# Optimization experiments

Hardware: AMD Instinct MI355X
Metric: run time of the kernel (lower is better)

Reference implementation:

```python
import math
import jax, jax.numpy as jnp
import numpy as np

B, NQ, NKV, D, H = 32, 512, 512, 1024, 8
DH = D // H              # 128
N_COLS = 512             # n + 1
D_COL = math.ceil(2 * math.log2(N_COLS))  # 18


def setup_inputs() -> dict:
    key = jax.random.key(0)
    ks = jax.random.split(key, 8)
    s = 0.02
    return {
        "x_q": jax.random.normal(ks[0], (B, NQ, D), jnp.float32),
        "x_kv": jax.random.normal(ks[1], (B, NKV, D), jnp.float32),
        # sym_weight=True => W_tail is W_head (shared)
        "W_head_w": jax.random.normal(ks[2], (D, D), jnp.float32) * s,
        "W_head_b": jnp.zeros((D,), jnp.float32),
        "W_v_w": jax.random.normal(ks[3], (D, D), jnp.float32) * s,
        "W_v_b": jnp.zeros((D,), jnp.float32),
        "W_out_w": jax.random.normal(ks[4], (D, D), jnp.float32) * s,
        "W_out_b": jnp.zeros((D,), jnp.float32),
        "rel_emb": jnp.ones((H, DH), jnp.float32),
        "col_head": jax.random.normal(ks[5], (H, N_COLS, D_COL), jnp.float32) * 0.2,
        "col_tail": jax.random.normal(ks[6], (H, N_COLS, D_COL), jnp.float32) * 0.2,
    }


def _heads(x, W, b, h, dh):
    # Linear then split heads: [B, n, d] -> [B, H, n, dh]
    B_, n, _ = x.shape
    y = x @ W.T + b
    return y.reshape(B_, n, h, dh).transpose(0, 2, 1, 3)


def reference(x_q, x_kv, W_head_w, W_head_b, W_v_w, W_v_b,
              W_out_w, W_out_b, rel_emb, col_head, col_tail):
    Bb, nq, d = x_q.shape
    nkv = x_kv.shape[1]
    h, dh = rel_emb.shape

    f_head = _heads(x_q, W_head_w, W_head_b, h, dh) * rel_emb[None, :, None, :]
    f_tail = _heads(x_kv, W_head_w, W_head_b, h, dh) * rel_emb[None, :, None, :]  # W_tail = W_head (sym_weight)
    f_v = _heads(x_kv, W_v_w, W_v_b, h, dh)

    # content score: [B, H, nq, nkv]
    weight_score = jnp.einsum('bhqd,bhkd->bhqk', f_head, f_tail) / math.sqrt(dh)

    # learned column topology: [H, n_cols, n_cols]
    adj_logits = jnp.einsum('hqc,hkc->hqk', col_head, col_tail)
    eye = jnp.eye(adj_logits.shape[-1], dtype=bool)  # nsi: zero diagonal before softmax
    adj_logits = jnp.where(eye[None], 0.0, adj_logits)
    adj = jax.nn.softmax(adj_logits, axis=-1)[:, :nq, :nkv]

    adj_mask = (1.0 - adj) * -10000.0
    fr_graph = jax.nn.softmax(weight_score + adj_mask[None], axis=-1)

    x = jnp.einsum('bhqk,bhkd->bhqd', fr_graph, f_v)
    x = x.transpose(0, 2, 1, 3).reshape(Bb, nq, h * dh)
    x = x @ W_out_w.T + W_out_b
    return (x, fr_graph.reshape(Bb * h, nq, nkv))
```

## Files before the change

kernel.cpp:

```cpp
#include <hip/hip_runtime.h>

typedef __attribute__((ext_vector_type(8))) __bf16 bf8;
typedef __attribute__((ext_vector_type(4))) __bf16 bf4;
typedef __attribute__((ext_vector_type(4))) float f32x4;

#define DEVI static __device__ __forceinline__

DEVI void gload_lds16(const void* g, void* l) {
  __builtin_amdgcn_global_load_lds(
      (const __attribute__((address_space(1))) unsigned int*)g,
      (__attribute__((address_space(3))) unsigned int*)l, 16, 0, 0);
}

#define WAITV(N)                                             \
  asm volatile("s_waitcnt vmcnt(" #N ")" ::: "memory");      \
  __builtin_amdgcn_sched_barrier(0)
#define BARRIER()                      \
  __builtin_amdgcn_sched_barrier(0);   \
  __builtin_amdgcn_s_barrier();        \
  __builtin_amdgcn_sched_barrier(0)

__global__ __launch_bounds__(256) void cvt_kernel(const float* __restrict__ in,
                                                  __bf16* __restrict__ out, int n4) {
  int stride = gridDim.x * blockDim.x;
  for (int i = blockIdx.x * blockDim.x + threadIdx.x; i < n4; i += stride) {
    f32x4 v = reinterpret_cast<const f32x4*>(in)[i];
    bf4 o;
    o[0] = (__bf16)v[0]; o[1] = (__bf16)v[1]; o[2] = (__bf16)v[2]; o[3] = (__bf16)v[3];
    reinterpret_cast<bf4*>(out)[i] = o;
  }
}

template <int MODE>
__global__ __launch_bounds__(512, 2) void gemm_proj(
    const __bf16* __restrict__ A, const __bf16* __restrict__ Bw,
    const float* __restrict__ bias, const float* __restrict__ rel,
    __bf16* __restrict__ obf, float* __restrict__ of32) {
  __shared__ alignas(16) __bf16 As0[256 * 64];
  __shared__ alignas(16) __bf16 Bs0[256 * 64];
  __shared__ alignas(16) __bf16 As1[256 * 64];
  __shared__ alignas(16) __bf16 Bs1[256 * 64];
  const int tid = threadIdx.x;
  const int lane = tid & 63;
  const int wave = tid >> 6;
  const int wr = wave >> 2;
  const int wc = wave & 3;
  const int lr = lane & 15;
  const int khi = lane >> 4;
  const int bm = blockIdx.x, bn = blockIdx.y;

  const __bf16* Ab = A + (size_t)bm * 256 * 1024;
  const __bf16* Bb = Bw + (size_t)bn * 256 * 1024;

  const int srow = tid >> 3;
  const int scc = (tid & 7) ^ (srow & 7);

  f32x4 acc[8][4];
#pragma unroll
  for (int mi = 0; mi < 8; ++mi)
#pragma unroll
    for (int ni = 0; ni < 4; ++ni)
#pragma unroll
      for (int e = 0; e < 4; ++e) acc[mi][ni][e] = 0.f;

  auto STAGE = [&](const __bf16* gb, __bf16* lds, int kt) {
#pragma unroll
    for (int i = 0; i < 4; ++i)
      gload_lds16(gb + (size_t)(i * 64 + srow) * 1024 + kt * 64 + scc * 8,
                  lds + i * 4096 + tid * 8);
  };

  auto COMPUTE = [&](const __bf16* As, const __bf16* Bs) {
    __builtin_amdgcn_s_setprio(1);
#pragma unroll
    for (int kk = 0; kk < 2; ++kk) {
      const int ck = ((kk * 4 + khi) ^ (lr & 7)) * 8;
      bf8 a[8], b[4];
#pragma unroll
      for (int mi = 0; mi < 8; ++mi)
        a[mi] = *reinterpret_cast<const bf8*>(&As[(wr * 128 + mi * 16 + lr) * 64 + ck]);
#pragma unroll
      for (int ni = 0; ni < 4; ++ni)
        b[ni] = *reinterpret_cast<const bf8*>(&Bs[(wc * 64 + ni * 16 + lr) * 64 + ck]);
#pragma unroll
      for (int mi = 0; mi < 8; ++mi)
#pragma unroll
        for (int ni = 0; ni < 4; ++ni)
          acc[mi][ni] = __builtin_amdgcn_mfma_f32_16x16x32_bf16(a[mi], b[ni], acc[mi][ni], 0, 0, 0);
    }
    __builtin_amdgcn_s_setprio(0);
  };

  STAGE(Ab, As0, 0); STAGE(Bb, Bs0, 0);
  STAGE(Ab, As1, 1); STAGE(Bb, Bs1, 1);

  for (int it = 0; it < 7; ++it) {
    WAITV(8);
    BARRIER();
    COMPUTE(As0, Bs0);
    BARRIER();
    STAGE(Ab, As0, 2 * it + 2); STAGE(Bb, Bs0, 2 * it + 2);
    WAITV(8);
    BARRIER();
    COMPUTE(As1, Bs1);
    BARRIER();
    STAGE(Ab, As1, 2 * it + 3); STAGE(Bb, Bs1, 2 * it + 3);
  }
  WAITV(8);
  BARRIER();
  COMPUTE(As0, Bs0);
  WAITV(0);
  BARRIER();
  COMPUTE(As1, Bs1);

#pragma unroll
  for (int mi = 0; mi < 8; ++mi) {
#pragma unroll
    for (int ni = 0; ni < 4; ++ni) {
      const int n = bn * 256 + wc * 64 + ni * 16 + lr;
#pragma unroll
      for (int r = 0; r < 4; ++r) {
        const int m = bm * 256 + wr * 128 + mi * 16 + khi * 4 + r;
        float v = acc[mi][ni][r] + bias[n];
        if (MODE == 0) v *= rel[n];
        if (MODE == 2) {
          of32[(size_t)m * 1024 + n] = v;
        } else if (MODE == 0) {
          size_t idx = ((size_t)((m >> 9) * 8 + (n >> 7))) * 65536 +
                       (size_t)(m & 511) * 128 + (n & 127);
          obf[idx] = (__bf16)v;
        } else {
          size_t idx = ((size_t)((m >> 9) * 8 + (n >> 7))) * 65536 +
                       (size_t)(n & 127) * 512 + (m & 511);
          obf[idx] = (__bf16)v;
        }
      }
    }
  }
}

__global__ __launch_bounds__(256) void adj_kernel(const float* __restrict__ ch_all,
                                                  const float* __restrict__ ct_all,
                                                  __bf16* __restrict__ adjT) {
  const int wave = threadIdx.x >> 6, lane = threadIdx.x & 63;
  const int row = blockIdx.x * 4 + wave;
  const int h = row >> 9, i = row & 511;
  float ch[18];
  const float* chp = ch_all + ((size_t)h * 512 + i) * 18;
#pragma unroll
  for (int t = 0; t < 18; ++t) ch[t] = chp[t];
  float e[8];
  float m = -1e30f;
#pragma unroll
  for (int jj = 0; jj < 8; ++jj) {
    const int j = jj * 64 + lane;
    const float* ctp = ct_all + ((size_t)h * 512 + j) * 18;
    float d = 0.f;
#pragma unroll
    for (int t = 0; t < 18; ++t) d += ch[t] * ctp[t];
    if (j == i) d = 0.f;
    e[jj] = d;
    m = fmaxf(m, d);
  }
#pragma unroll
  for (int off = 32; off >= 1; off >>= 1) m = fmaxf(m, __shfl_xor(m, off));
  float s = 0.f;
#pragma unroll
  for (int jj = 0; jj < 8; ++jj) { e[jj] = __expf(e[jj] - m); s += e[jj]; }
#pragma unroll
  for (int off = 32; off >= 1; off >>= 1) s += __shfl_xor(s, off);
  const float inv = 10000.f / s;
  __bf16* op = adjT + (size_t)h * 262144 + i;
#pragma unroll
  for (int jj = 0; jj < 8; ++jj)
    op[(size_t)(jj * 64 + lane) * 512] = (__bf16)(e[jj] * inv - 19.53125f);
}

__global__ __launch_bounds__(256, 3) void fused_attn_kernel(
    const __bf16* __restrict__ fh, const __bf16* __restrict__ ft,
    const __bf16* __restrict__ fvT, const __bf16* __restrict__ adjT,
    float* __restrict__ fr, __bf16* __restrict__ ctx) {
  __shared__ alignas(16) __bf16 Bt[128 * 128];
  __shared__ alignas(16) __bf16 Pl[4][16 * 128];
  const int tid = threadIdx.x;
  const int l = tid & 63, w = tid >> 6;
  const int b = blockIdx.x;
  const int h = blockIdx.y >> 3;
  const int qt = blockIdx.y & 7;
  const int bh = b * 8 + h;
  const int wrow = qt * 64 + w * 16;
  const int lr = l & 15;
  const int khi = l >> 4;

  const int srow = tid >> 4;
  const int scc = (tid & 15) ^ (srow & 7);

  bf8 afr[4];
  {
    const __bf16* ap = fh + (size_t)bh * 65536 + (size_t)(wrow + lr) * 128 + khi * 8;
#pragma unroll
    for (int kk4 = 0; kk4 < 4; ++kk4)
      afr[kk4] = *reinterpret_cast<const bf8*>(ap + kk4 * 32);
  }

  f32x4 acc[32];
#pragma unroll
  for (int n = 0; n < 32; ++n)
#pragma unroll
    for (int e = 0; e < 4; ++e) acc[n][e] = 0.f;

  const __bf16* ftb = ft + (size_t)bh * 65536;
#pragma unroll
  for (int kt = 0; kt < 4; ++kt) {
#pragma unroll
    for (int i = 0; i < 8; ++i)
      gload_lds16(ftb + (size_t)(kt * 128 + i * 16 + srow) * 128 + scc * 8,
                  Bt + i * 2048 + tid * 8);
    __syncthreads();
    __builtin_amdgcn_s_setprio(1);
#pragma unroll
    for (int kk4 = 0; kk4 < 4; ++kk4) {
      bf8 bfr[8];
#pragma unroll
      for (int n2 = 0; n2 < 8; ++n2)
        bfr[n2] = *reinterpret_cast<const bf8*>(
            &Bt[(n2 * 16 + lr) * 128 + ((kk4 * 4 + khi) ^ (lr & 7)) * 8]);
#pragma unroll
      for (int n2 = 0; n2 < 8; ++n2)
        acc[kt * 8 + n2] =
            __builtin_amdgcn_mfma_f32_16x16x32_bf16(afr[kk4], bfr[n2], acc[kt * 8 + n2], 0, 0, 0);
    }
    __builtin_amdgcn_s_setprio(0);
    __syncthreads();
  }

  const float scale = 0.08838834764831845f;
  const __bf16* adjTp = adjT + (size_t)h * 262144;
  float mrow[4] = {-1e30f, -1e30f, -1e30f, -1e30f};
#pragma unroll
  for (int n = 0; n < 32; ++n) {
    const int col = n * 16 + lr;
    bf4 av4 = *reinterpret_cast<const bf4*>(adjTp + (size_t)col * 512 + wrow + khi * 4);
#pragma unroll
    for (int r = 0; r < 4; ++r) {
      float v = acc[n][r] * scale + (float)av4[r];
      acc[n][r] = v;
      mrow[r] = fmaxf(mrow[r], v);
    }
  }
#pragma unroll
  for (int r = 0; r < 4; ++r)
#pragma unroll
    for (int off = 1; off <= 8; off <<= 1) mrow[r] = fmaxf(mrow[r], __shfl_xor(mrow[r], off));
  float srw[4] = {0.f, 0.f, 0.f, 0.f};
#pragma unroll
  for (int n = 0; n < 32; ++n)
#pragma unroll
    for (int r = 0; r < 4; ++r) {
      float e = __expf(acc[n][r] - mrow[r]);
      acc[n][r] = e;
      srw[r] += e;
    }
#pragma unroll
  for (int r = 0; r < 4; ++r)
#pragma unroll
    for (int off = 1; off <= 8; off <<= 1) srw[r] += __shfl_xor(srw[r], off);
  float inv[4];
#pragma unroll
  for (int r = 0; r < 4; ++r) inv[r] = 1.f / srw[r];
#pragma unroll
  for (int n = 0; n < 32; ++n)
#pragma unroll
    for (int r = 0; r < 4; ++r) acc[n][r] *= inv[r];

  const __bf16* fvb = fvT + (size_t)bh * 65536;
#pragma unroll
  for (int i = 0; i < 8; ++i)
    gload_lds16(fvb + (size_t)(i * 16 + srow) * 512 + scc * 8, Bt + i * 2048 + tid * 8);

  {
    float* frb = fr + (size_t)bh * 262144;
#pragma unroll
    for (int n = 0; n < 32; ++n) {
      const int col = n * 16 + lr;
#pragma unroll
      for (int r = 0; r < 4; ++r)
        frb[(size_t)(wrow + khi * 4 + r) * 512 + col] = acc[n][r];
    }
  }

  f32x4 acc2[8];
#pragma unroll
  for (int n2 = 0; n2 < 8; ++n2)
#pragma unroll
    for (int e = 0; e < 4; ++e) acc2[n2][e] = 0.f;

  __bf16* Pw = &Pl[w][0];
#pragma unroll
  for (int kt = 0; kt < 4; ++kt) {
#pragma unroll
    for (int n2 = 0; n2 < 8; ++n2) {
      const int colc = n2 * 2 + (lr >> 3);
      const int cl = lr & 7;
#pragma unroll
      for (int r = 0; r < 4; ++r) {
        const int q = khi * 4 + r;
        Pw[q * 128 + ((colc ^ (q & 7)) * 8) + cl] = (__bf16)acc[kt * 8 + n2][r];
      }
    }
    __syncthreads();
    __builtin_amdgcn_s_setprio(1);
#pragma unroll
    for (int kk4 = 0; kk4 < 4; ++kk4) {
      bf8 pa = *reinterpret_cast<const bf8*>(
          &Pw[lr * 128 + ((kk4 * 4 + khi) ^ (lr & 7)) * 8]);
      bf8 bfr[8];
#pragma unroll
      for (int n2 = 0; n2 < 8; ++n2)
        bfr[n2] = *reinterpret_cast<const bf8*>(
            &Bt[(n2 * 16 + lr) * 128 + ((kk4 * 4 + khi) ^ (lr & 7)) * 8]);
#pragma unroll
      for (int n2 = 0; n2 < 8; ++n2)
        acc2[n2] = __builtin_amdgcn_mfma_f32_16x16x32_bf16(pa, bfr[n2], acc2[n2], 0, 0, 0);
    }
    __builtin_amdgcn_s_setprio(0);
    __syncthreads();
    if (kt < 3) {
      const int ktn = kt + 1;
#pragma unroll
      for (int i = 0; i < 8; ++i)
        gload_lds16(fvb + (size_t)(i * 16 + srow) * 512 + ktn * 128 + scc * 8,
                    Bt + i * 2048 + tid * 8);
    }
  }

#pragma unroll
  for (int n2 = 0; n2 < 8; ++n2) {
    const int c = n2 * 16 + lr;
#pragma unroll
    for (int r = 0; r < 4; ++r) {
      const int q = wrow + khi * 4 + r;
      ctx[(size_t)(b * 512 + q) * 1024 + h * 128 + c] = (__bf16)acc2[n2][r];
    }
  }
}

extern "C" void kernel_launch(void* const* d_in, const int* in_sizes, int n_in,
                              void* d_out, int out_size, void* d_ws, size_t ws_size,
                              hipStream_t stream) {
  const float* x_q  = (const float*)d_in[0];
  const float* x_kv = (const float*)d_in[1];
  const float* Wh   = (const float*)d_in[2];
  const float* bh   = (const float*)d_in[3];
  const float* Wv   = (const float*)d_in[4];
  const float* bv   = (const float*)d_in[5];
  const float* Wo   = (const float*)d_in[6];
  const float* bo   = (const float*)d_in[7];
  const float* rel  = (const float*)d_in[8];
  const float* colh = (const float*)d_in[9];
  const float* colt = (const float*)d_in[10];

  float* out = (float*)d_out;
  float* fr  = out + 16777216;

  __bf16* xq_bf  = (__bf16*)d_ws;
  __bf16* xkv_bf = xq_bf + 16777216;
  __bf16* Wh_bf  = xkv_bf + 16777216;
  __bf16* Wv_bf  = Wh_bf + 1048576;
  __bf16* Wo_bf  = Wv_bf + 1048576;
  __bf16* fhead  = Wo_bf + 1048576;
  __bf16* ftail  = fhead + 16777216;
  __bf16* fvT    = ftail + 16777216;
  __bf16* adjT   = fvT + 16777216;
  __bf16* ctx    = adjT + 2097152;

  cvt_kernel<<<4096, 256, 0, stream>>>(x_q, xq_bf, 4194304);
  cvt_kernel<<<4096, 256, 0, stream>>>(x_kv, xkv_bf, 4194304);
  cvt_kernel<<<1024, 256, 0, stream>>>(Wh, Wh_bf, 262144);
  cvt_kernel<<<1024, 256, 0, stream>>>(Wv, Wv_bf, 262144);
  cvt_kernel<<<1024, 256, 0, stream>>>(Wo, Wo_bf, 262144);

  dim3 gp(64, 4);
  gemm_proj<0><<<gp, 512, 0, stream>>>(xq_bf, Wh_bf, bh, rel, fhead, nullptr);
  gemm_proj<0><<<gp, 512, 0, stream>>>(xkv_bf, Wh_bf, bh, rel, ftail, nullptr);
  gemm_proj<1><<<gp, 512, 0, stream>>>(xkv_bf, Wv_bf, bv, nullptr, fvT, nullptr);

  adj_kernel<<<1024, 256, 0, stream>>>(colh, colt, adjT);

  fused_attn_kernel<<<dim3(32, 64), 256, 0, stream>>>(fhead, ftail, fvT, adjT, fr, ctx);

  gemm_proj<2><<<gp, 512, 0, stream>>>(ctx, Wo_bf, bo, nullptr, nullptr, out);
}
```

Measured before the change: 817.1 us.

## Double-buffer LDS staging of K and V tiles in fused attention kernel

Splits the single shared-memory tile into two buffers. Each K/V tile load is issued one stage ahead, and the first V tiles are prefetched during the QK^T loop. Full `__syncthreads` calls are replaced with explicit vmcnt/lgkmcnt waits and barriers, so global-to-LDS copies overlap MFMA work. This costs extra LDS, which cuts the launch-bounds occupancy target from 3 to 2 blocks per CU. The vmcnt waits also now cover the fr output stores issued before the PV loop.

```diff
diff --git a/kernel.cpp b/kernel.cpp
--- a/kernel.cpp
+++ b/kernel.cpp
@@ -14,6 +14,9 @@
 
 #define WAITV(N)                                             \
   asm volatile("s_waitcnt vmcnt(" #N ")" ::: "memory");      \
+  __builtin_amdgcn_sched_barrier(0)
+#define LGKM0()                                              \
+  asm volatile("s_waitcnt lgkmcnt(0)" ::: "memory");         \
   __builtin_amdgcn_sched_barrier(0)
 #define BARRIER()                      \
   __builtin_amdgcn_sched_barrier(0);   \
@@ -176,11 +179,12 @@
     op[(size_t)(jj * 64 + lane) * 512] = (__bf16)(e[jj] * inv - 19.53125f);
 }
 
-__global__ __launch_bounds__(256, 3) void fused_attn_kernel(
+__global__ __launch_bounds__(256, 2) void fused_attn_kernel(
     const __bf16* __restrict__ fh, const __bf16* __restrict__ ft,
     const __bf16* __restrict__ fvT, const __bf16* __restrict__ adjT,
     float* __restrict__ fr, __bf16* __restrict__ ctx) {
-  __shared__ alignas(16) __bf16 Bt[128 * 128];
+  __shared__ alignas(16) __bf16 Bt0[128 * 128];
+  __shared__ alignas(16) __bf16 Bt1[128 * 128];
   __shared__ alignas(16) __bf16 Pl[4][16 * 128];
   const int tid = threadIdx.x;
   const int l = tid & 63, w = tid >> 6;
@@ -203,20 +207,35 @@
       afr[kk4] = *reinterpret_cast<const bf8*>(ap + kk4 * 32);
   }
 
-  f32x4 acc[32];
-#pragma unroll
-  for (int n = 0; n < 32; ++n)
-#pragma unroll
-    for (int e = 0; e < 4; ++e) acc[n][e] = 0.f;
-
   const __bf16* ftb = ft + (size_t)bh * 65536;
-#pragma unroll
-  for (int kt = 0; kt < 4; ++kt) {
+  const __bf16* fvb = fvT + (size_t)bh * 65536;
+
+  auto stage_ft = [&](__bf16* dst, int kt) {
 #pragma unroll
     for (int i = 0; i < 8; ++i)
       gload_lds16(ftb + (size_t)(kt * 128 + i * 16 + srow) * 128 + scc * 8,
-                  Bt + i * 2048 + tid * 8);
-    __syncthreads();
+                  dst + i * 2048 + tid * 8);
+  };
+  auto stage_fv = [&](__bf16* dst, int kt) {
+#pragma unroll
+    for (int i = 0; i < 8; ++i)
+      gload_lds16(fvb + (size_t)(i * 16 + srow) * 512 + kt * 128 + scc * 8,
+                  dst + i * 2048 + tid * 8);
+  };
+
+  f32x4 acc[32];
+#pragma unroll
+  for (int n = 0; n < 32; ++n)
+#pragma unroll
+    for (int e = 0; e < 4; ++e) acc[n][e] = 0.f;
+
+  stage_ft(Bt0, 0);
+  stage_ft(Bt1, 1);
+#pragma unroll
+  for (int kt = 0; kt < 4; ++kt) {
+    __bf16* B = (kt & 1) ? Bt1 : Bt0;
+    WAITV(8);
+    BARRIER();
     __builtin_amdgcn_s_setprio(1);
 #pragma unroll
     for (int kk4 = 0; kk4 < 4; ++kk4) {
@@ -224,14 +243,18 @@
 #pragma unroll
       for (int n2 = 0; n2 < 8; ++n2)
         bfr[n2] = *reinterpret_cast<const bf8*>(
-            &Bt[(n2 * 16 + lr) * 128 + ((kk4 * 4 + khi) ^ (lr & 7)) * 8]);
+            &B[(n2 * 16 + lr) * 128 + ((kk4 * 4 + khi) ^ (lr & 7)) * 8]);
 #pragma unroll
       for (int n2 = 0; n2 < 8; ++n2)
         acc[kt * 8 + n2] =
             __builtin_amdgcn_mfma_f32_16x16x32_bf16(afr[kk4], bfr[n2], acc[kt * 8 + n2], 0, 0, 0);
     }
     __builtin_amdgcn_s_setprio(0);
-    __syncthreads();
+    BARRIER();
+    if (kt == 0) stage_ft(Bt0, 2);
+    else if (kt == 1) stage_ft(Bt1, 3);
+    else if (kt == 2) stage_fv(Bt0, 0);
+    else stage_fv(Bt1, 1);
   }
 
   const float scale = 0.08838834764831845f;
@@ -273,11 +296,6 @@
 #pragma unroll
     for (int r = 0; r < 4; ++r) acc[n][r] *= inv[r];
 
-  const __bf16* fvb = fvT + (size_t)bh * 65536;
-#pragma unroll
-  for (int i = 0; i < 8; ++i)
-    gload_lds16(fvb + (size_t)(i * 16 + srow) * 512 + scc * 8, Bt + i * 2048 + tid * 8);
-
   {
     float* frb = fr + (size_t)bh * 262144;
 #pragma unroll
@@ -298,6 +316,7 @@
   __bf16* Pw = &Pl[w][0];
 #pragma unroll
   for (int kt = 0; kt < 4; ++kt) {
+    __bf16* B = (kt & 1) ? Bt1 : Bt0;
 #pragma unroll
     for (int n2 = 0; n2 < 8; ++n2) {
       const int colc = n2 * 2 + (lr >> 3);
@@ -308,7 +327,9 @@
         Pw[q * 128 + ((colc ^ (q & 7)) * 8) + cl] = (__bf16)acc[kt * 8 + n2][r];
       }
     }
-    __syncthreads();
+    LGKM0();
+    if (kt < 3) { WAITV(8); } else { WAITV(0); }
+    BARRIER();
     __builtin_amdgcn_s_setprio(1);
 #pragma unroll
     for (int kk4 = 0; kk4 < 4; ++kk4) {
@@ -318,19 +339,16 @@
 #pragma unroll
       for (int n2 = 0; n2 < 8; ++n2)
         bfr[n2] = *reinterpret_cast<const bf8*>(
-            &Bt[(n2 * 16 + lr) * 128 + ((kk4 * 4 + khi) ^ (lr & 7)) * 8]);
+            &B[(n2 * 16 + lr) * 128 + ((kk4 * 4 + khi) ^ (lr & 7)) * 8]);
 #pragma unroll
       for (int n2 = 0; n2 < 8; ++n2)
         acc2[n2] = __builtin_amdgcn_mfma_f32_16x16x32_bf16(pa, bfr[n2], acc2[n2], 0, 0, 0);
     }
     __builtin_amdgcn_s_setprio(0);
-    __syncthreads();
     if (kt < 3) {
-      const int ktn = kt + 1;
-#pragma unroll
-      for (int i = 0; i < 8; ++i)
-        gload_lds16(fvb + (size_t)(i * 16 + srow) * 512 + ktn * 128 + scc * 8,
-                    Bt + i * 2048 + tid * 8);
+      BARRIER();
+      if (kt == 0) stage_fv(Bt0, 2);
+      else if (kt == 1) stage_fv(Bt1, 3);
     }
   }
 
```

Measured after the change: 726.8 us. 11.1% less time.
